# Performance work log

Measured on AMD Instinct MI355X. Metric: run time of the kernel, lower is better.

The kernel has to match this reference:

```python
import jax, jax.numpy as jnp
import numpy as np
import math

L, B, T, D, H, DH, DM, V = 4, 1, 2048, 1024, 16, 64, 4096, 32000
K_TOP = 512
EPS = 1e-6


def setup_inputs() -> dict:
    key = jax.random.key(0)
    ks = jax.random.split(key, 8)
    s = 0.02
    sp = 0.02 / math.sqrt(2 * L)  # c_proj special init
    return {
        "idx": jax.random.randint(ks[0], (B, T), 0, V),
        "wte": jax.random.normal(ks[1], (V, D), jnp.float32) * s,
        "wpe": jax.random.normal(ks[2], (T, D), jnp.float32) * s,
        "ln1_w": jnp.ones((L, D), jnp.float32),
        "ln2_w": jnp.ones((L, D), jnp.float32),
        "W_attn": jax.random.normal(ks[3], (L, D, 3 * H * DH), jnp.float32) * s,
        "W_attn_proj": jax.random.normal(ks[4], (L, H * DH, D), jnp.float32) * sp,
        "W_fc": jax.random.normal(ks[5], (L, D, DM), jnp.float32) * s,
        "W_mlp_proj": jax.random.normal(ks[6], (L, DM, D), jnp.float32) * sp,
        "sink_logit": jnp.zeros((L, H), jnp.float32),
        "lnf_w": jnp.ones((D,), jnp.float32),
        "lm_head_w": jax.random.normal(ks[7], (D, V), jnp.float32) * s,
        "k_topk": K_TOP,
    }


def rmsnorm(x, w):
    return x * jax.lax.rsqrt(jnp.mean(x * x, axis=-1, keepdims=True) + EPS) * w


def abs_topk(x, k):
    # zero all but the k largest-magnitude entries along the last axis
    if k >= x.shape[-1]:
        return x
    vals = jax.lax.top_k(jnp.abs(x), k)[0]
    thresh = vals[..., -1:]
    return jnp.where(jnp.abs(x) >= thresh, x, jnp.zeros((), x.dtype))


def attention_with_sink(xn, Wa, Wap, sink, causal):
    b, t, _ = xn.shape
    qkv = xn @ Wa  # [B,T,3*H*DH]
    q, k, v = jnp.split(qkv, 3, axis=-1)
    q = q.reshape(b, t, H, DH).transpose(0, 2, 1, 3)  # [B,H,T,DH]
    k = k.reshape(b, t, H, DH).transpose(0, 2, 1, 3)
    v = v.reshape(b, t, H, DH).transpose(0, 2, 1, 3)
    scale = 1.0 / math.sqrt(DH)
    scores = jnp.einsum('bhqd,bhkd->bhqk', q, k) * scale
    neg = jnp.finfo(scores.dtype).min
    scores = jnp.where(causal, scores, neg)
    # sink: zero key/value slot at position 0, logit = per-head learnable bias
    sink_col = jnp.broadcast_to(sink[None, :, None, None], (b, H, t, 1)).astype(scores.dtype)
    logits = jnp.concatenate([sink_col, scores], axis=-1)  # [B,H,T,T+1]
    probs = jax.nn.softmax(logits, axis=-1)
    y = jnp.einsum('bhqk,bhkd->bhqd', probs[..., 1:], v)  # sink v is zero
    y = y.transpose(0, 2, 1, 3).reshape(b, t, H * DH)
    return y @ Wap


def reference(idx, wte, wpe, ln1_w, ln2_w, W_attn, W_attn_proj, W_fc, W_mlp_proj,
              sink_logit, lnf_w, lm_head_w, k_topk):
    b, t = idx.shape
    x = wte[idx] + wpe[jnp.arange(t)][None]  # [B,T,D]
    causal = jnp.tril(jnp.ones((t, t), bool))

    def block(x, p):
        l1, l2, Wa, Wap, Wf, Wp, sk = p
        x = x + attention_with_sink(rmsnorm(x, l1), Wa, Wap, sk, causal)
        h = jax.nn.gelu(rmsnorm(x, l2) @ Wf, approximate=False)
        h = abs_topk(h, k_topk)  # AbsTopK at 'mlp_neuron'
        x = x + h @ Wp
        return x, None

    x, _ = jax.lax.scan(block, x, (ln1_w, ln2_w, W_attn, W_attn_proj, W_fc, W_mlp_proj, sink_logit))
    return rmsnorm(x, lnf_w) @ lm_head_w  # [B,T,V]
```

## Files before the change

kernel.cpp:

```cpp
#include <hip/hip_runtime.h>


typedef unsigned int u32;

#define TT 2048
#define DD 1024
#define HH 16
#define DMM 4096
#define VV 32000
#define AQ 4

__global__ __launch_bounds__(256) void embed32_k(const int* __restrict__ idx,
    const float* __restrict__ wte, const float* __restrict__ wpe, float* __restrict__ x){
  int t = blockIdx.x, tid = threadIdx.x;
  int tok = idx[t];
  #pragma unroll
  for (int i=0;i<4;i++){
    int e = tid*4 + i;
    x[(size_t)t*DD + e] = __fadd_rn(wte[(size_t)tok*DD + e], wpe[(size_t)t*DD + e]);
  }
}

__global__ __launch_bounds__(64) void rms_xla_k(const float* __restrict__ x,
    const float* __restrict__ w, float* __restrict__ out){
  __shared__ float sq[1024];
  __shared__ float p5[512];
  __shared__ float fin[64];
  __shared__ float srt;
  int row = blockIdx.x, lane = threadIdx.x;
  const float* xr = x + (size_t)row*DD;
  for (int i=lane; i<1024; i+=64){ float v = xr[i]; sq[i] = __fmul_rn(v,v); }
  __syncthreads();
  for (int t=lane; t<512; t+=64)
    p5[t] = __fadd_rn(sq[2*t], sq[2*t+1]);
  __syncthreads();
  #pragma unroll
  for (int off=32; off; off>>=1){
    for (int t=lane; t<8*off; t+=64){
      int wv = t/off, ii = t - wv*off;
      p5[64*wv+ii] = __fadd_rn(p5[64*wv+ii], p5[64*wv+ii+off]);
    }
    __syncthreads();
  }
  fin[lane] = (lane<8) ? p5[64*lane] : 0.0f;
  __syncthreads();
  #pragma unroll
  for (int off=32; off; off>>=1){
    if (lane<off) fin[lane] = __fadd_rn(fin[lane], fin[lane+off]);
    __syncthreads();
  }
  if (lane==0){
    float mean = __fdiv_rn(fin[0], 1024.0f);
    srt = rsqrtf(__fadd_rn(mean, 1e-6f));
  }
  __syncthreads();
  float r = srt;
  for (int i=lane; i<1024; i+=64)
    out[(size_t)row*DD + i] = __fmul_rn(__fmul_rn(xr[i], r), w[i]);
}

template<int MODE, int NQ>
__global__ __launch_bounds__(256) void gemm_fast_k(const float* __restrict__ A,
    const float* __restrict__ B, float* __restrict__ C, int M, int N, int K){
  __shared__ float As[32][132];
  __shared__ float Bs[32][64*NQ+4];
  const int tid = threadIdx.x;
  const int tr = tid >> 4, tc = tid & 15;
  const int m0 = blockIdx.y*128, n0 = blockIdx.x*(64*NQ);

  float acc[8][4*NQ];
  #pragma unroll
  for (int i=0;i<8;i++)
    #pragma unroll
    for (int j=0;j<4*NQ;j++) acc[i][j] = 0.0f;

  for (int kk=0; kk<K; kk+=32){
    __syncthreads();
    #pragma unroll
    for (int it=0; it<4; ++it){
      int id = it*256 + tid;
      int row = id >> 3, f4 = id & 7;
      float4 v = *(const float4*)&A[(size_t)(m0+row)*K + kk + 4*f4];
      As[4*f4+0][row] = v.x; As[4*f4+1][row] = v.y;
      As[4*f4+2][row] = v.z; As[4*f4+3][row] = v.w;
    }
    #pragma unroll
    for (int it=0; it<2*NQ; ++it){
      int id = it*256 + tid;
      int r = id / (16*NQ), f4 = id % (16*NQ);
      *(float4*)&Bs[r][4*f4] = *(const float4*)&B[(size_t)(kk+r)*N + n0 + 4*f4];
    }
    __syncthreads();
    #pragma unroll 4
    for (int k=0; k<32; ++k){
      float4 a0 = *(const float4*)&As[k][4*tr];
      float4 a1 = *(const float4*)&As[k][64 + 4*tr];
      float av[8] = {a0.x,a0.y,a0.z,a0.w, a1.x,a1.y,a1.z,a1.w};
      float bv[4*NQ];
      {
        float4 b0 = *(const float4*)&Bs[k][4*tc];
        bv[0]=b0.x; bv[1]=b0.y; bv[2]=b0.z; bv[3]=b0.w;
        if (NQ==2){
          float4 b1 = *(const float4*)&Bs[k][64 + 4*tc];
          bv[4]=b1.x; bv[5]=b1.y; bv[6]=b1.z; bv[7]=b1.w;
        }
      }
      #pragma unroll
      for (int i=0;i<8;i++)
        #pragma unroll
        for (int j=0;j<4*NQ;j++)
          acc[i][j] = __builtin_fmaf(av[i], bv[j], acc[i][j]);
    }
  }
  #pragma unroll
  for (int i=0;i<8;i++){
    int row = m0 + (i>>2)*64 + 4*tr + (i&3);
    #pragma unroll
    for (int jq=0;jq<NQ;jq++){
      size_t off = (size_t)row*N + n0 + jq*64 + 4*tc;
      #pragma unroll
      for (int e=0;e<4;e++){
        float vv = acc[i][jq*4+e];
        if (MODE==0){
          C[off+e] = vv;
        } else if (MODE==1){
          C[off+e] = __fadd_rn(C[off+e], vv);
        } else {
          float t = __fdiv_rn(vv, 1.41421356f);
          float g = erff(t);
          C[off+e] = __fmul_rn(__fmul_rn(0.5f, vv), __fadd_rn(1.0f, g));
        }
      }
    }
  }
}

__global__ __launch_bounds__(256) void attn_v3_k(const float* __restrict__ qkv,
    const float* __restrict__ sink, float* __restrict__ y){
  __shared__ float arr[AQ][2049];
  __shared__ float Qs[AQ][64];
  __shared__ float p5[AQ][512];
  __shared__ float fin[AQ][64];
  __shared__ float wmax[4][AQ];
  __shared__ float mq[AQ];
  __shared__ float dq[AQ];
  const int tid = threadIdx.x;
  const int lane = tid & 63, wvv = tid >> 6;
  const int h = blockIdx.y, q0 = blockIdx.x*AQ;
  const int qmax = q0 + AQ - 1;
  const float snk = sink[h];

  if (tid < AQ*64)
    Qs[tid>>6][tid&63] = qkv[(size_t)(q0 + (tid>>6))*3072 + h*64 + (tid&63)];
  __syncthreads();

  float sc[AQ][9];
  float ml[AQ];
  #pragma unroll
  for (int qi=0;qi<AQ;qi++) ml[qi] = -3.402823466e38f;

  #pragma unroll
  for (int k=0;k<9;k++){
    int s = tid + 256*k;
    #pragma unroll
    for (int qi=0;qi<AQ;qi++) sc[qi][k] = 0.0f;
    if (s >= 1 && s < 2049){
      int kv = s - 1;
      if (kv <= qmax){
        const float* kr = qkv + (size_t)kv*3072 + 1024 + h*64;
        float da[AQ];
        #pragma unroll
        for (int qi=0;qi<AQ;qi++) da[qi] = 0.0f;
        #pragma unroll 2
        for (int d0=0; d0<64; d0+=8){
          float4 ka = *(const float4*)&kr[d0];
          float4 kb = *(const float4*)&kr[d0+4];
          float kvv[8] = {ka.x,ka.y,ka.z,ka.w, kb.x,kb.y,kb.z,kb.w};
          #pragma unroll
          for (int qi=0;qi<AQ;qi++)
            #pragma unroll
            for (int e=0;e<8;e++)
              da[qi] = __builtin_fmaf(Qs[qi][d0+e], kvv[e], da[qi]);
        }
        #pragma unroll
        for (int qi=0;qi<AQ;qi++){
          float sv = __fmul_rn(da[qi], 0.125f);
          sc[qi][k] = sv;
          if (kv <= q0+qi) ml[qi] = fmaxf(ml[qi], sv);
        }
      }
    }
  }

  #pragma unroll
  for (int qi=0;qi<AQ;qi++){
    float m = ml[qi];
    #pragma unroll
    for (int off=1; off<64; off<<=1) m = fmaxf(m, __shfl_xor(m, off, 64));
    if (lane==0) wmax[wvv][qi] = m;
  }
  __syncthreads();
  if (tid < AQ){
    float m = fmaxf(fmaxf(wmax[0][tid], wmax[1][tid]),
                    fmaxf(wmax[2][tid], wmax[3][tid]));
    mq[tid] = fmaxf(m, snk);
  }
  __syncthreads();

  #pragma unroll
  for (int k=0;k<9;k++){
    int s = tid + 256*k;
    #pragma unroll
    for (int qi=0;qi<AQ;qi++){
      bool valid = (s>=1) && (s<2049) && (s-1 <= q0+qi);
      sc[qi][k] = valid ? expf(__fsub_rn(sc[qi][k], mq[qi])) : 0.0f;
    }
  }
  if (tid==0){
    #pragma unroll
    for (int qi=0;qi<AQ;qi++) sc[qi][0] = expf(__fsub_rn(snk, mq[qi]));
  }

  #pragma unroll
  for (int qi=0;qi<AQ;qi++){
    float pe = 0.0f, po = 0.0f;
    #pragma unroll
    for (int k=0;k<9;k+=2) if (tid + 256*k < 2049) pe = __fadd_rn(pe, sc[qi][k]);
    #pragma unroll
    for (int k=1;k<9;k+=2) if (tid + 256*k < 2049) po = __fadd_rn(po, sc[qi][k]);
    p5[qi][tid]       = pe;
    p5[qi][tid + 256] = po;
  }
  __syncthreads();
  #pragma unroll
  for (int off=32; off; off>>=1){
    for (int t=tid; t<AQ*8*off; t+=256){
      int qi = t/(8*off); int rem = t - qi*8*off;
      int g = rem/off, ii = rem - g*off;
      p5[qi][64*g+ii] = __fadd_rn(p5[qi][64*g+ii], p5[qi][64*g+ii+off]);
    }
    __syncthreads();
  }
  { int qi = tid>>6, i = tid&63; fin[qi][i] = (i<8) ? p5[qi][64*i] : 0.0f; }
  __syncthreads();
  #pragma unroll
  for (int off=32; off; off>>=1){
    for (int t=tid; t<AQ*off; t+=256){
      int qi = t/off, ii = t - qi*off;
      fin[qi][ii] = __fadd_rn(fin[qi][ii], fin[qi][ii+off]);
    }
    __syncthreads();
  }
  if (tid < AQ) dq[tid] = fin[tid][0];
  __syncthreads();

  #pragma unroll
  for (int k=0;k<9;k++){
    int s = tid + 256*k;
    if (s >= 1 && s < 2049){
      #pragma unroll
      for (int qi=0;qi<AQ;qi++)
        arr[qi][s] = (s-1 <= q0+qi) ? __fdiv_rn(sc[qi][k], dq[qi]) : 0.0f;
    }
  }
  __syncthreads();

  const int qi = wvv, d = lane;
  const int qa = q0 + qi;
  float acc = 0.0f;
  const float* vb = qkv + 2048 + h*64 + d;
  int kv = 0;
  for (; kv + 8 <= qa + 1; kv += 8){
    #pragma unroll
    for (int e=0;e<8;e++)
      acc = __builtin_fmaf(arr[qi][1+kv+e], vb[(size_t)(kv+e)*3072], acc);
  }
  for (; kv <= qa; ++kv)
    acc = __builtin_fmaf(arr[qi][1+kv], vb[(size_t)kv*3072], acc);
  y[(size_t)qa*DD + h*64 + d] = acc;
}

__global__ __launch_bounds__(256) void topk32_k(float* __restrict__ h,
    const int* __restrict__ kptr){
  const int row = blockIdx.x, tid = threadIdx.x;
  __shared__ int suf[256];
  __shared__ int s_sel, s_k;
  float* hr = h + (size_t)row*DMM;
  int kk = kptr[0];
  u32 prefix = 0u;
  for (int pass=0; pass<4; pass++){
    int shift = 24 - 8*pass;
    u32 hi_mask = pass ? (0xFFFFFFFFu << (shift+8)) : 0u;
    suf[tid] = 0;
    __syncthreads();
    for (int i=0;i<16;i++){
      u32 b = __float_as_uint(hr[tid + 256*i]) & 0x7fffffffu;
      if ((b & hi_mask) == prefix) atomicAdd(&suf[(b>>shift)&255], 1);
    }
    __syncthreads();
    for (int s=1;s<256;s<<=1){
      int v2 = (tid+s<256) ? suf[tid+s] : 0;
      __syncthreads();
      suf[tid] += v2;
      __syncthreads();
    }
    int nxt = (tid<255) ? suf[tid+1] : 0;
    if (suf[tid] >= kk && nxt < kk){ s_sel = tid; s_k = kk - nxt; }
    __syncthreads();
    prefix |= ((u32)s_sel) << shift;
    kk = s_k;
    __syncthreads();
  }
  for (int i=0;i<16;i++){
    int e = tid + 256*i;
    u32 b = __float_as_uint(hr[e]) & 0x7fffffffu;
    if (b < prefix) hr[e] = 0.0f;
  }
}

extern "C" void kernel_launch(void* const* d_in, const int* in_sizes, int n_in,
                              void* d_out, int out_size, void* d_ws, size_t ws_size,
                              hipStream_t stream){
  const int*   idx  = (const int*)  d_in[0];
  const float* wte  = (const float*)d_in[1];
  const float* wpe  = (const float*)d_in[2];
  const float* ln1  = (const float*)d_in[3];
  const float* ln2  = (const float*)d_in[4];
  const float* Wa   = (const float*)d_in[5];
  const float* Wap  = (const float*)d_in[6];
  const float* Wf   = (const float*)d_in[7];
  const float* Wp   = (const float*)d_in[8];
  const float* sink = (const float*)d_in[9];
  const float* lnf  = (const float*)d_in[10];
  const float* lmw  = (const float*)d_in[11];
  const int*   kptr = (const int*)  d_in[12];
  (void)in_sizes; (void)n_in; (void)out_size; (void)ws_size;

  char* w = (char*)d_ws;
  float* x   = (float*)(w);
  float* xn  = (float*)(w + 8388608);
  float* qkv = (float*)(w + 16777216);
  float* y   = (float*)(w + 41943040);
  float* h   = (float*)(w + 50331648);

  embed32_k<<<TT, 256, 0, stream>>>(idx, wte, wpe, x);

  for (int l=0; l<4; l++){
    rms_xla_k<<<TT, 64, 0, stream>>>(x, ln1 + l*DD, xn);
    gemm_fast_k<0,2><<<dim3(3072/128, TT/128), 256, 0, stream>>>(xn, Wa + (size_t)l*1024*3072, qkv, TT, 3072, 1024);
    attn_v3_k<<<dim3(TT/AQ, HH), 256, 0, stream>>>(qkv, sink + l*HH, y);
    gemm_fast_k<1,1><<<dim3(1024/64, TT/128), 256, 0, stream>>>(y, Wap + (size_t)l*1024*1024, x, TT, 1024, 1024);
    rms_xla_k<<<TT, 64, 0, stream>>>(x, ln2 + l*DD, xn);
    gemm_fast_k<2,2><<<dim3(4096/128, TT/128), 256, 0, stream>>>(xn, Wf + (size_t)l*1024*4096, h, TT, 4096, 1024);
    topk32_k<<<TT, 256, 0, stream>>>(h, kptr);
    gemm_fast_k<1,1><<<dim3(1024/64, TT/128), 256, 0, stream>>>(h, Wp + (size_t)l*4096*1024, x, TT, 1024, 4096);
  }

  rms_xla_k<<<TT, 64, 0, stream>>>(x, lnf, xn);
  gemm_fast_k<0,2><<<dim3(VV/128, TT/128), 256, 0, stream>>>(xn, lmw, (float*)d_out, TT, VV, 1024);
}
```

Baseline: 8.875 ms.

## Double-buffer GEMM shared tiles and stage K tiles in LDS for attention

The GEMM now uses two 16-deep shared-memory buffers and prefetches the next A/B tile into registers while computing the current one. This overlaps global loads with FMAs and needs one barrier per iteration instead of two. The attention kernel is restructured so each wave owns one query held in registers. Keys are loaded in 64-row tiles into LDS and shared across the block, replacing the earlier per-thread global K reads, and scores go straight into the shared probability array. The trade-off is more registers (64-float q vector, prefetch registers) and a smaller K-step per barrier.

```diff
diff --git a/kernel.cpp b/kernel.cpp
--- a/kernel.cpp
+++ b/kernel.cpp
@@ -60,50 +60,68 @@
 }
 
 template<int MODE, int NQ>
-__global__ __launch_bounds__(256) void gemm_fast_k(const float* __restrict__ A,
+__global__ __launch_bounds__(256) void gemm_db_k(const float* __restrict__ A,
     const float* __restrict__ B, float* __restrict__ C, int M, int N, int K){
-  __shared__ float As[32][132];
-  __shared__ float Bs[32][64*NQ+4];
+  __shared__ float As[2][16][132];
+  __shared__ float Bs[2][16][64*NQ+4];
   const int tid = threadIdx.x;
   const int tr = tid >> 4, tc = tid & 15;
   const int m0 = blockIdx.y*128, n0 = blockIdx.x*(64*NQ);
 
+  const int ar0 = tid >> 2,       af0 = tid & 3;
+  const int ar1 = (256+tid) >> 2, af1 = tid & 3;
   float acc[8][4*NQ];
   #pragma unroll
   for (int i=0;i<8;i++)
     #pragma unroll
     for (int j=0;j<4*NQ;j++) acc[i][j] = 0.0f;
 
-  for (int kk=0; kk<K; kk+=32){
-    __syncthreads();
-    #pragma unroll
-    for (int it=0; it<4; ++it){
-      int id = it*256 + tid;
-      int row = id >> 3, f4 = id & 7;
-      float4 v = *(const float4*)&A[(size_t)(m0+row)*K + kk + 4*f4];
-      As[4*f4+0][row] = v.x; As[4*f4+1][row] = v.y;
-      As[4*f4+2][row] = v.z; As[4*f4+3][row] = v.w;
-    }
-    #pragma unroll
-    for (int it=0; it<2*NQ; ++it){
-      int id = it*256 + tid;
-      int r = id / (16*NQ), f4 = id % (16*NQ);
-      *(float4*)&Bs[r][4*f4] = *(const float4*)&B[(size_t)(kk+r)*N + n0 + 4*f4];
-    }
-    __syncthreads();
+  const int niter = K >> 4;
+  {
+    float4 va0 = *(const float4*)&A[(size_t)(m0+ar0)*K + 4*af0];
+    float4 va1 = *(const float4*)&A[(size_t)(m0+ar1)*K + 4*af1];
+    As[0][4*af0+0][ar0]=va0.x; As[0][4*af0+1][ar0]=va0.y; As[0][4*af0+2][ar0]=va0.z; As[0][4*af0+3][ar0]=va0.w;
+    As[0][4*af1+0][ar1]=va1.x; As[0][4*af1+1][ar1]=va1.y; As[0][4*af1+2][ar1]=va1.z; As[0][4*af1+3][ar1]=va1.w;
+    if (NQ==2){
+      int r0 = tid>>5, c40 = tid&31;
+      int r1 = (256+tid)>>5, c41 = tid&31;
+      *(float4*)&Bs[0][r0][4*c40] = *(const float4*)&B[(size_t)r0*N + n0 + 4*c40];
+      *(float4*)&Bs[0][r1][4*c41] = *(const float4*)&B[(size_t)r1*N + n0 + 4*c41];
+    } else {
+      int r0 = tid>>4, c40 = tid&15;
+      *(float4*)&Bs[0][r0][4*c40] = *(const float4*)&B[(size_t)r0*N + n0 + 4*c40];
+    }
+  }
+  __syncthreads();
+
+  for (int t=0; t<niter; ++t){
+    const int cur = t & 1;
+    float4 va0, va1, vb0, vb1;
+    if (t+1 < niter){
+      int kk = (t+1) << 4;
+      va0 = *(const float4*)&A[(size_t)(m0+ar0)*K + kk + 4*af0];
+      va1 = *(const float4*)&A[(size_t)(m0+ar1)*K + kk + 4*af1];
+      if (NQ==2){
+        int r0 = tid>>5, c40 = tid&31;
+        int r1 = (256+tid)>>5;
+        vb0 = *(const float4*)&B[(size_t)(kk+r0)*N + n0 + 4*c40];
+        vb1 = *(const float4*)&B[(size_t)(kk+r1)*N + n0 + 4*c40];
+      } else {
+        int r0 = tid>>4, c40 = tid&15;
+        vb0 = *(const float4*)&B[(size_t)(kk+r0)*N + n0 + 4*c40];
+      }
+    }
     #pragma unroll 4
-    for (int k=0; k<32; ++k){
-      float4 a0 = *(const float4*)&As[k][4*tr];
-      float4 a1 = *(const float4*)&As[k][64 + 4*tr];
+    for (int k=0; k<16; ++k){
+      float4 a0 = *(const float4*)&As[cur][k][4*tr];
+      float4 a1 = *(const float4*)&As[cur][k][64 + 4*tr];
+      float4 b0 = *(const float4*)&Bs[cur][k][4*tc];
       float av[8] = {a0.x,a0.y,a0.z,a0.w, a1.x,a1.y,a1.z,a1.w};
       float bv[4*NQ];
-      {
-        float4 b0 = *(const float4*)&Bs[k][4*tc];
-        bv[0]=b0.x; bv[1]=b0.y; bv[2]=b0.z; bv[3]=b0.w;
-        if (NQ==2){
-          float4 b1 = *(const float4*)&Bs[k][64 + 4*tc];
-          bv[4]=b1.x; bv[5]=b1.y; bv[6]=b1.z; bv[7]=b1.w;
-        }
+      bv[0]=b0.x; bv[1]=b0.y; bv[2]=b0.z; bv[3]=b0.w;
+      if (NQ==2){
+        float4 b1 = *(const float4*)&Bs[cur][k][64 + 4*tc];
+        bv[4]=b1.x; bv[5]=b1.y; bv[6]=b1.z; bv[7]=b1.w;
       }
       #pragma unroll
       for (int i=0;i<8;i++)
@@ -111,7 +129,23 @@
         for (int j=0;j<4*NQ;j++)
           acc[i][j] = __builtin_fmaf(av[i], bv[j], acc[i][j]);
     }
-  }
+    if (t+1 < niter){
+      const int nxt = cur ^ 1;
+      As[nxt][4*af0+0][ar0]=va0.x; As[nxt][4*af0+1][ar0]=va0.y; As[nxt][4*af0+2][ar0]=va0.z; As[nxt][4*af0+3][ar0]=va0.w;
+      As[nxt][4*af1+0][ar1]=va1.x; As[nxt][4*af1+1][ar1]=va1.y; As[nxt][4*af1+2][ar1]=va1.z; As[nxt][4*af1+3][ar1]=va1.w;
+      if (NQ==2){
+        int r0 = tid>>5, c40 = tid&31;
+        int r1 = (256+tid)>>5;
+        *(float4*)&Bs[nxt][r0][4*c40] = vb0;
+        *(float4*)&Bs[nxt][r1][4*c40] = vb1;
+      } else {
+        int r0 = tid>>4, c40 = tid&15;
+        *(float4*)&Bs[nxt][r0][4*c40] = vb0;
+      }
+    }
+    __syncthreads();
+  }
+
   #pragma unroll
   for (int i=0;i<8;i++){
     int row = m0 + (i>>2)*64 + 4*tr + (i&3);
@@ -126,8 +160,8 @@
         } else if (MODE==1){
           C[off+e] = __fadd_rn(C[off+e], vv);
         } else {
-          float t = __fdiv_rn(vv, 1.41421356f);
-          float g = erff(t);
+          float t2 = __fdiv_rn(vv, 1.41421356f);
+          float g = erff(t2);
           C[off+e] = __fmul_rn(__fmul_rn(0.5f, vv), __fadd_rn(1.0f, g));
         }
       }
@@ -135,101 +169,87 @@
   }
 }
 
-__global__ __launch_bounds__(256) void attn_v3_k(const float* __restrict__ qkv,
+__global__ __launch_bounds__(256) void attn_v5_k(const float* __restrict__ qkv,
     const float* __restrict__ sink, float* __restrict__ y){
-  __shared__ float arr[AQ][2049];
-  __shared__ float Qs[AQ][64];
-  __shared__ float p5[AQ][512];
-  __shared__ float fin[AQ][64];
-  __shared__ float wmax[4][AQ];
+  __shared__ float arr[AQ][2052];
+  __shared__ float uks[64*68];
   __shared__ float mq[AQ];
   __shared__ float dq[AQ];
+  float (*Ks)[68]   = (float(*)[68])uks;
+  float (*p5)[512]  = (float(*)[512])uks;
+  float (*fin)[64]  = (float(*)[64])(uks + AQ*512);
   const int tid = threadIdx.x;
-  const int lane = tid & 63, wvv = tid >> 6;
+  const int lane = tid & 63, wv = tid >> 6;
   const int h = blockIdx.y, q0 = blockIdx.x*AQ;
+  const int qa_w = q0 + wv;
+  const float snk = sink[h];
+
+  #pragma unroll
+  for (int qi=0;qi<AQ;qi++)
+    for (int s=tid; s<2052; s+=256) arr[qi][s] = 0.0f;
+
+  float qv[64];
+  {
+    const float* qr = qkv + (size_t)qa_w*3072 + h*64;
+    #pragma unroll
+    for (int c4=0;c4<16;c4++){
+      float4 v = *(const float4*)&qr[4*c4];
+      qv[4*c4]=v.x; qv[4*c4+1]=v.y; qv[4*c4+2]=v.z; qv[4*c4+3]=v.w;
+    }
+  }
+
+  float ml = -3.402823466e38f;
   const int qmax = q0 + AQ - 1;
-  const float snk = sink[h];
-
-  if (tid < AQ*64)
-    Qs[tid>>6][tid&63] = qkv[(size_t)(q0 + (tid>>6))*3072 + h*64 + (tid&63)];
-  __syncthreads();
-
-  float sc[AQ][9];
-  float ml[AQ];
-  #pragma unroll
-  for (int qi=0;qi<AQ;qi++) ml[qi] = -3.402823466e38f;
-
-  #pragma unroll
-  for (int k=0;k<9;k++){
-    int s = tid + 256*k;
-    #pragma unroll
-    for (int qi=0;qi<AQ;qi++) sc[qi][k] = 0.0f;
-    if (s >= 1 && s < 2049){
-      int kv = s - 1;
-      if (kv <= qmax){
-        const float* kr = qkv + (size_t)kv*3072 + 1024 + h*64;
-        float da[AQ];
-        #pragma unroll
-        for (int qi=0;qi<AQ;qi++) da[qi] = 0.0f;
-        #pragma unroll 2
-        for (int d0=0; d0<64; d0+=8){
-          float4 ka = *(const float4*)&kr[d0];
-          float4 kb = *(const float4*)&kr[d0+4];
-          float kvv[8] = {ka.x,ka.y,ka.z,ka.w, kb.x,kb.y,kb.z,kb.w};
-          #pragma unroll
-          for (int qi=0;qi<AQ;qi++)
-            #pragma unroll
-            for (int e=0;e<8;e++)
-              da[qi] = __builtin_fmaf(Qs[qi][d0+e], kvv[e], da[qi]);
-        }
-        #pragma unroll
-        for (int qi=0;qi<AQ;qi++){
-          float sv = __fmul_rn(da[qi], 0.125f);
-          sc[qi][k] = sv;
-          if (kv <= q0+qi) ml[qi] = fmaxf(ml[qi], sv);
-        }
-      }
-    }
-  }
+  for (int base=0; base<=qmax; base+=64){
+    __syncthreads();
+    #pragma unroll
+    for (int it=0; it<4; ++it){
+      int id = it*256 + tid;
+      int r = id >> 4, c4 = id & 15;
+      int kr = base + r;
+      if (kr < TT)
+        *(float4*)&Ks[r][4*c4] = *(const float4*)&qkv[(size_t)kr*3072 + 1024 + h*64 + 4*c4];
+    }
+    __syncthreads();
+    int kv = base + lane;
+    if (kv <= qa_w){
+      float s = 0.0f;
+      #pragma unroll
+      for (int c4=0;c4<16;c4++){
+        float4 kf = *(const float4*)&Ks[lane][4*c4];
+        s = __builtin_fmaf(qv[4*c4  ], kf.x, s);
+        s = __builtin_fmaf(qv[4*c4+1], kf.y, s);
+        s = __builtin_fmaf(qv[4*c4+2], kf.z, s);
+        s = __builtin_fmaf(qv[4*c4+3], kf.w, s);
+      }
+      s = __fmul_rn(s, 0.125f);
+      arr[wv][1+kv] = s;
+      ml = fmaxf(ml, s);
+    }
+  }
+  #pragma unroll
+  for (int off=1; off<64; off<<=1) ml = fmaxf(ml, __shfl_xor(ml, off, 64));
+  if (lane==0) mq[wv] = fmaxf(ml, snk);
+  __syncthreads();
 
   #pragma unroll
   for (int qi=0;qi<AQ;qi++){
-    float m = ml[qi];
-    #pragma unroll
-    for (int off=1; off<64; off<<=1) m = fmaxf(m, __shfl_xor(m, off, 64));
-    if (lane==0) wmax[wvv][qi] = m;
-  }
-  __syncthreads();
-  if (tid < AQ){
-    float m = fmaxf(fmaxf(wmax[0][tid], wmax[1][tid]),
-                    fmaxf(wmax[2][tid], wmax[3][tid]));
-    mq[tid] = fmaxf(m, snk);
-  }
-  __syncthreads();
-
-  #pragma unroll
-  for (int k=0;k<9;k++){
-    int s = tid + 256*k;
-    #pragma unroll
-    for (int qi=0;qi<AQ;qi++){
-      bool valid = (s>=1) && (s<2049) && (s-1 <= q0+qi);
-      sc[qi][k] = valid ? expf(__fsub_rn(sc[qi][k], mq[qi])) : 0.0f;
-    }
-  }
-  if (tid==0){
-    #pragma unroll
-    for (int qi=0;qi<AQ;qi++) sc[qi][0] = expf(__fsub_rn(snk, mq[qi]));
-  }
-
-  #pragma unroll
-  for (int qi=0;qi<AQ;qi++){
-    float pe = 0.0f, po = 0.0f;
-    #pragma unroll
-    for (int k=0;k<9;k+=2) if (tid + 256*k < 2049) pe = __fadd_rn(pe, sc[qi][k]);
-    #pragma unroll
-    for (int k=1;k<9;k+=2) if (tid + 256*k < 2049) po = __fadd_rn(po, sc[qi][k]);
-    p5[qi][tid]       = pe;
-    p5[qi][tid + 256] = po;
+    float m = mq[qi]; int qa = q0+qi;
+    for (int s=tid; s<2049; s+=256){
+      if (s >= 1 && s-1 <= qa)
+        arr[qi][s] = expf(__fsub_rn(arr[qi][s], m));
+    }
+  }
+  if (tid < AQ) arr[tid][0] = expf(__fsub_rn(snk, mq[tid]));
+  __syncthreads();
+
+  #pragma unroll
+  for (int m2=0; m2<8; ++m2){
+    int flat = m2*256 + tid;
+    int qi = flat >> 9, t = flat & 511;
+    float a = 0.0f;
+    for (int s=t; s<2049; s+=512) a = __fadd_rn(a, arr[qi][s]);
+    p5[qi][t] = a;
   }
   __syncthreads();
   #pragma unroll
@@ -255,29 +275,26 @@
   __syncthreads();
 
   #pragma unroll
-  for (int k=0;k<9;k++){
-    int s = tid + 256*k;
-    if (s >= 1 && s < 2049){
-      #pragma unroll
-      for (int qi=0;qi<AQ;qi++)
-        arr[qi][s] = (s-1 <= q0+qi) ? __fdiv_rn(sc[qi][k], dq[qi]) : 0.0f;
-    }
-  }
-  __syncthreads();
-
-  const int qi = wvv, d = lane;
-  const int qa = q0 + qi;
+  for (int qi=0;qi<AQ;qi++){
+    float den = dq[qi]; int qa = q0+qi;
+    for (int s=tid; s<2049; s+=256)
+      if (s >= 1 && s-1 <= qa)
+        arr[qi][s] = __fdiv_rn(arr[qi][s], den);
+  }
+  __syncthreads();
+
+  const int d = lane;
   float acc = 0.0f;
   const float* vb = qkv + 2048 + h*64 + d;
   int kv = 0;
-  for (; kv + 8 <= qa + 1; kv += 8){
+  for (; kv + 8 <= qa_w + 1; kv += 8){
     #pragma unroll
     for (int e=0;e<8;e++)
-      acc = __builtin_fmaf(arr[qi][1+kv+e], vb[(size_t)(kv+e)*3072], acc);
-  }
-  for (; kv <= qa; ++kv)
-    acc = __builtin_fmaf(arr[qi][1+kv], vb[(size_t)kv*3072], acc);
-  y[(size_t)qa*DD + h*64 + d] = acc;
+      acc = __builtin_fmaf(arr[wv][1+kv+e], vb[(size_t)(kv+e)*3072], acc);
+  }
+  for (; kv <= qa_w; ++kv)
+    acc = __builtin_fmaf(arr[wv][1+kv], vb[(size_t)kv*3072], acc);
+  y[(size_t)qa_w*DD + h*64 + d] = acc;
 }
 
 __global__ __launch_bounds__(256) void topk32_k(float* __restrict__ h,
@@ -347,15 +364,15 @@
 
   for (int l=0; l<4; l++){
     rms_xla_k<<<TT, 64, 0, stream>>>(x, ln1 + l*DD, xn);
-    gemm_fast_k<0,2><<<dim3(3072/128, TT/128), 256, 0, stream>>>(xn, Wa + (size_t)l*1024*3072, qkv, TT, 3072, 1024);
-    attn_v3_k<<<dim3(TT/AQ, HH), 256, 0, stream>>>(qkv, sink + l*HH, y);
-    gemm_fast_k<1,1><<<dim3(1024/64, TT/128), 256, 0, stream>>>(y, Wap + (size_t)l*1024*1024, x, TT, 1024, 1024);
+    gemm_db_k<0,2><<<dim3(3072/128, TT/128), 256, 0, stream>>>(xn, Wa + (size_t)l*1024*3072, qkv, TT, 3072, 1024);
+    attn_v5_k<<<dim3(TT/AQ, HH), 256, 0, stream>>>(qkv, sink + l*HH, y);
+    gemm_db_k<1,1><<<dim3(1024/64, TT/128), 256, 0, stream>>>(y, Wap + (size_t)l*1024*1024, x, TT, 1024, 1024);
     rms_xla_k<<<TT, 64, 0, stream>>>(x, ln2 + l*DD, xn);
-    gemm_fast_k<2,2><<<dim3(4096/128, TT/128), 256, 0, stream>>>(xn, Wf + (size_t)l*1024*4096, h, TT, 4096, 1024);
+    gemm_db_k<2,2><<<dim3(4096/128, TT/128), 256, 0, stream>>>(xn, Wf + (size_t)l*1024*4096, h, TT, 4096, 1024);
     topk32_k<<<TT, 256, 0, stream>>>(h, kptr);
-    gemm_fast_k<1,1><<<dim3(1024/64, TT/128), 256, 0, stream>>>(h, Wp + (size_t)l*4096*1024, x, TT, 1024, 4096);
+    gemm_db_k<1,1><<<dim3(1024/64, TT/128), 256, 0, stream>>>(h, Wp + (size_t)l*4096*1024, x, TT, 1024, 4096);
   }
 
   rms_xla_k<<<TT, 64, 0, stream>>>(x, lnf, xn);
-  gemm_fast_k<0,2><<<dim3(VV/128, TT/128), 256, 0, stream>>>(xn, lmw, (float*)d_out, TT, VV, 1024);
-}
+  gemm_db_k<0,2><<<dim3(VV/128, TT/128), 256, 0, stream>>>(xn, lmw, (float*)d_out, TT, VV, 1024);
+}
```

After: 8.001 ms. -9.8%, faster.
